# Optimization experiments

Measured on AMD Instinct MI355X. Metric: run time of the kernel, lower is better.

Reference implementation:

```python
import jax, jax.numpy as jnp
import numpy as np

# Fixed genome topology (layered DAG, topologically ordered levels)
B = 4096      # batch
N_IN = 512    # input nodes
H1 = 1536     # hidden level 1
H2 = 1536     # hidden level 2
N_OUT = 512   # output nodes
FAN = 32      # fan-in per non-input node


def setup_inputs() -> dict:
    key = jax.random.key(0)
    ks = jax.random.split(key, 10)
    x = jax.random.normal(ks[0], (B, N_IN), dtype=jnp.float32)
    # level 1: sources among inputs [0, N_IN)
    src0 = jax.random.randint(ks[1], (H1 * FAN,), 0, N_IN, dtype=jnp.int32)
    dst0 = jax.random.randint(ks[2], (H1 * FAN,), 0, H1, dtype=jnp.int32)
    w0 = jax.random.normal(ks[3], (H1 * FAN,), dtype=jnp.float32) * 0.1
    # level 2: sources among inputs + level1 [0, N_IN+H1)
    src1 = jax.random.randint(ks[4], (H2 * FAN,), 0, N_IN + H1, dtype=jnp.int32)
    dst1 = jax.random.randint(ks[5], (H2 * FAN,), 0, H2, dtype=jnp.int32)
    w1 = jax.random.normal(ks[6], (H2 * FAN,), dtype=jnp.float32) * 0.1
    # output level: sources among all earlier nodes [0, N_IN+H1+H2)
    src2 = jax.random.randint(ks[7], (N_OUT * FAN,), 0, N_IN + H1 + H2, dtype=jnp.int32)
    dst2 = jax.random.randint(ks[8], (N_OUT * FAN,), 0, N_OUT, dtype=jnp.int32)
    w2 = jax.random.normal(ks[9], (N_OUT * FAN,), dtype=jnp.float32) * 0.1
    return dict(x=x, src0=src0, dst0=dst0, w0=w0,
                src1=src1, dst1=dst1, w1=w1,
                src2=src2, dst2=dst2, w2=w2)


def _level(node_values, src, dst, w, size):
    # per-edge weighted gather: [B, E]
    vals = node_values[:, src] * w
    # scatter-add into destination nodes of this level: [B, size]
    agg = jnp.zeros((node_values.shape[0], size), node_values.dtype).at[:, dst].add(vals)
    # per-node activation (genome.activation == 'relu'); relu(0)=0 matches
    # original's behavior of leaving unconnected nodes at zero
    return jax.nn.relu(agg)


def reference(x, src0, dst0, w0, src1, dst1, w1, src2, dst2, w2):
    nv = x                                        # [B, N_IN]
    h1 = _level(nv, src0, dst0, w0, H1)           # [B, H1]
    nv = jnp.concatenate([nv, h1], axis=1)        # [B, N_IN+H1]
    h2 = _level(nv, src1, dst1, w1, H2)           # [B, H2]
    nv = jnp.concatenate([nv, h2], axis=1)        # [B, N_IN+H1+H2]
    out = _level(nv, src2, dst2, w2, N_OUT)       # [B, N_OUT]
    return out
```

## Files before the change

kernel.cpp:

```cpp
#include <hip/hip_runtime.h>
#include <hip/hip_fp16.h>
#include <stdint.h>

#define BATCH 4096
#define N_IN  512
#define H1    1536
#define H2    1536
#define N_OUT 512
#define FAN   32
#define E0 (H1 * FAN)
#define E1 (H2 * FAN)
#define E2 (N_OUT * FAN)
#define ETOT (E0 + E1 + E2)
#define NNODES (H1 + H2 + N_OUT)
#define MAXDEG 128

#define ROWU4 520
#define ROWH  (ROWU4 * 8)

#define OFF_EDGES 34078720
#define OFF_CNT   (OFF_EDGES + NNODES * MAXDEG * 8)

__global__ __launch_bounds__(256) void k_transpose_in(const float* __restrict__ x,
                                                      __half* __restrict__ xT) {
    __shared__ float tile[32][33];
    const int tx = threadIdx.x, ty = threadIdx.y;
    const int n0 = blockIdx.x * 32;
    const int b0 = blockIdx.y * 32;
#pragma unroll
    for (int k = 0; k < 32; k += 8)
        tile[ty + k][tx] = x[(size_t)(b0 + ty + k) * N_IN + (n0 + tx)];
    __syncthreads();
#pragma unroll
    for (int k = 0; k < 32; k += 8)
        xT[(size_t)(n0 + ty + k) * ROWH + (b0 + tx)] = __float2half_rn(tile[tx][ty + k]);
}

__global__ __launch_bounds__(256) void k_fill(const int* __restrict__ s0, const int* __restrict__ d0, const float* __restrict__ w0,
                                              const int* __restrict__ s1, const int* __restrict__ d1, const float* __restrict__ w1,
                                              const int* __restrict__ s2, const int* __restrict__ d2, const float* __restrict__ w2,
                                              int* __restrict__ cnt, int2* __restrict__ edges) {
    const int e = blockIdx.x * 256 + threadIdx.x;
    int src, node; float w;
    if (e < E0)           { src = s0[e];          node = d0[e];                w = w0[e]; }
    else if (e < E0 + E1) { int i = e - E0;       src = s1[i]; node = H1 + d1[i];        w = w1[i]; }
    else                  { int i = e - E0 - E1;  src = s2[i]; node = H1 + H2 + d2[i];   w = w2[i]; }
    const int pos = atomicAdd(&cnt[node], 1);
    if (pos < MAXDEG) edges[node * MAXDEG + pos] = make_int2(src, __float_as_int(w));
}

__global__ __launch_bounds__(256, 8)
void k_level(const int2* __restrict__ edges,
             const int* __restrict__ cnt,
             const uint4* __restrict__ nv,
             uint4* __restrict__ outb) {
    const int lane = threadIdx.x & 63;
    const int wv   = threadIdx.x >> 6;
    const int node = __builtin_amdgcn_readfirstlane((blockIdx.y << 2) | wv);
    const int col8 = (blockIdx.x << 6) | lane;

    int c = cnt[node];
    c = (c < 0) ? 0 : (c > MAXDEG ? MAXDEG : c);

    float a0 = 0.f, a1 = 0.f, a2 = 0.f, a3 = 0.f, a4 = 0.f, a5 = 0.f, a6 = 0.f, a7 = 0.f;

#define ACC8(q, W) {                                                    \
    const __half2 h0 = *(const __half2*)&(q).x;                         \
    const __half2 h1 = *(const __half2*)&(q).y;                         \
    const __half2 h2 = *(const __half2*)&(q).z;                         \
    const __half2 h3 = *(const __half2*)&(q).w;                         \
    a0 = fmaf(__low2float(h0),  (W), a0);                               \
    a1 = fmaf(__high2float(h0), (W), a1);                               \
    a2 = fmaf(__low2float(h1),  (W), a2);                               \
    a3 = fmaf(__high2float(h1), (W), a3);                               \
    a4 = fmaf(__low2float(h2),  (W), a4);                               \
    a5 = fmaf(__high2float(h2), (W), a5);                               \
    a6 = fmaf(__low2float(h3),  (W), a6);                               \
    a7 = fmaf(__high2float(h3), (W), a7); }

    for (int base = 0; base < c; base += 64) {
        const int2 my = edges[(size_t)node * MAXDEG + base + lane];
        const int m = (c - base < 64) ? (c - base) : 64;
        int j = 0;
        for (; j + 4 <= m; j += 4) {
            const int   s0i = __builtin_amdgcn_readlane(my.x, j)     & 4095;
            const int   s1i = __builtin_amdgcn_readlane(my.x, j + 1) & 4095;
            const int   s2i = __builtin_amdgcn_readlane(my.x, j + 2) & 4095;
            const int   s3i = __builtin_amdgcn_readlane(my.x, j + 3) & 4095;
            const float wa  = __int_as_float(__builtin_amdgcn_readlane(my.y, j));
            const float wb  = __int_as_float(__builtin_amdgcn_readlane(my.y, j + 1));
            const float wc  = __int_as_float(__builtin_amdgcn_readlane(my.y, j + 2));
            const float wd  = __int_as_float(__builtin_amdgcn_readlane(my.y, j + 3));
            const uint4 q0 = nv[(size_t)s0i * ROWU4 + col8];
            const uint4 q1 = nv[(size_t)s1i * ROWU4 + col8];
            const uint4 q2 = nv[(size_t)s2i * ROWU4 + col8];
            const uint4 q3 = nv[(size_t)s3i * ROWU4 + col8];
            ACC8(q0, wa);
            ACC8(q1, wb);
            ACC8(q2, wc);
            ACC8(q3, wd);
        }
        for (; j < m; ++j) {
            const int   s0i = __builtin_amdgcn_readlane(my.x, j) & 4095;
            const float wa  = __int_as_float(__builtin_amdgcn_readlane(my.y, j));
            const uint4 q0 = nv[(size_t)s0i * ROWU4 + col8];
            ACC8(q0, wa);
        }
    }
#undef ACC8

    a0 = fmaxf(a0, 0.f); a1 = fmaxf(a1, 0.f); a2 = fmaxf(a2, 0.f); a3 = fmaxf(a3, 0.f);
    a4 = fmaxf(a4, 0.f); a5 = fmaxf(a5, 0.f); a6 = fmaxf(a6, 0.f); a7 = fmaxf(a7, 0.f);

    const __half2 h0 = __floats2half2_rn(a0, a1);
    const __half2 h1 = __floats2half2_rn(a2, a3);
    const __half2 h2 = __floats2half2_rn(a4, a5);
    const __half2 h3 = __floats2half2_rn(a6, a7);
    uint4 p;
    p.x = *(const uint32_t*)&h0; p.y = *(const uint32_t*)&h1;
    p.z = *(const uint32_t*)&h2; p.w = *(const uint32_t*)&h3;
    outb[(size_t)node * ROWU4 + col8] = p;
}

__global__ __launch_bounds__(256) void k_transpose_out(const __half* __restrict__ outh,
                                                       float* __restrict__ out) {
    __shared__ float tile[32][33];
    const int tx = threadIdx.x, ty = threadIdx.y;
    const int n0 = blockIdx.x * 32;
    const int b0 = blockIdx.y * 32;
#pragma unroll
    for (int k = 0; k < 32; k += 8)
        tile[ty + k][tx] = __half2float(outh[(size_t)(n0 + ty + k) * ROWH + (b0 + tx)]);
    __syncthreads();
#pragma unroll
    for (int k = 0; k < 32; k += 8)
        out[(size_t)(b0 + ty + k) * N_OUT + (n0 + tx)] = tile[tx][ty + k];
}

extern "C" void kernel_launch(void* const* d_in, const int* in_sizes, int n_in,
                              void* d_out, int out_size, void* d_ws, size_t ws_size,
                              hipStream_t stream) {
    const float* x  = (const float*)d_in[0];
    const int* s0   = (const int*)d_in[1];
    const int* dd0  = (const int*)d_in[2];
    const float* w0 = (const float*)d_in[3];
    const int* s1   = (const int*)d_in[4];
    const int* dd1  = (const int*)d_in[5];
    const float* w1 = (const float*)d_in[6];
    const int* s2   = (const int*)d_in[7];
    const int* dd2  = (const int*)d_in[8];
    const float* w2 = (const float*)d_in[9];

    char* ws        = (char*)d_ws;
    uint4*    nv4   = (uint4*)ws;
    int2*     edges = (int2*)(ws + OFF_EDGES);
    int*      cnt   = (int*)(ws + OFF_CNT);

    hipMemsetAsync(cnt, 0, NNODES * sizeof(int), stream);
    k_fill<<<ETOT / 256, 256, 0, stream>>>(s0, dd0, w0, s1, dd1, w1, s2, dd2, w2, cnt, edges);

    k_transpose_in<<<dim3(N_IN / 32, BATCH / 32), dim3(32, 8), 0, stream>>>(x, (__half*)ws);

    k_level<<<dim3(8, H1 / 4), 256, 0, stream>>>(edges, cnt, nv4,
                                                 nv4 + (size_t)N_IN * ROWU4);
    k_level<<<dim3(8, H2 / 4), 256, 0, stream>>>(edges + (size_t)H1 * MAXDEG, cnt + H1, nv4,
                                                 nv4 + (size_t)(N_IN + H1) * ROWU4);
    k_level<<<dim3(8, N_OUT / 4), 256, 0, stream>>>(edges + (size_t)(H1 + H2) * MAXDEG, cnt + H1 + H2, nv4,
                                                    nv4 + (size_t)(N_IN + H1 + H2) * ROWU4);

    k_transpose_out<<<dim3(N_OUT / 32, BATCH / 32), dim3(32, 8), 0, stream>>>(
        (const __half*)(ws + (size_t)(N_IN + H1 + H2) * ROWH * 2), (float*)d_out);
}
```

Measured before the change: 145.5 us.

## Stream gathered node rows through LDS with async global_load_lds pipeline

Replaces the direct per-edge register gathers in the level kernel with asynchronous global-to-LDS loads, one LDS slot per in-flight edge, four edges deep. Each edge is consumed after a manual vmcnt wait and its slot is refilled right away, so gather latency overlaps with the FMA work. Edges beyond the first 64, and any remainder not divisible by 4, fall back to plain scalar loads. The risks are the hand-written waitcnt correctness, extra LDS traffic, and the serial tail loop.

```diff
diff --git a/kernel.cpp b/kernel.cpp
--- a/kernel.cpp
+++ b/kernel.cpp
@@ -54,6 +54,7 @@
              const int* __restrict__ cnt,
              const uint4* __restrict__ nv,
              uint4* __restrict__ outb) {
+    __shared__ uint4 sh[4][4][64];
     const int lane = threadIdx.x & 63;
     const int wv   = threadIdx.x >> 6;
     const int node = __builtin_amdgcn_readfirstlane((blockIdx.y << 2) | wv);
@@ -78,35 +79,62 @@
     a6 = fmaf(__low2float(h3),  (W), a6);                               \
     a7 = fmaf(__high2float(h3), (W), a7); }
 
-    for (int base = 0; base < c; base += 64) {
-        const int2 my = edges[(size_t)node * MAXDEG + base + lane];
-        const int m = (c - base < 64) ? (c - base) : 64;
+#define GLD(K, SRC)                                                                   \
+    __builtin_amdgcn_global_load_lds(                                                 \
+        (const __attribute__((address_space(1))) void*)(const void*)                  \
+            (nv + (size_t)(SRC) * ROWU4 + col8),                                      \
+        (__attribute__((address_space(3))) void*)(void*)(&sh[wv][K][0]), 16, 0, 0)
+
+#define CONS(K, J, WAITSTR) {                                                         \
+    asm volatile(WAITSTR ::: "memory");                                               \
+    __builtin_amdgcn_sched_barrier(0);                                                \
+    const uint4 q = sh[wv][K][lane];                                                  \
+    const float w = __int_as_float(__builtin_amdgcn_readlane(my.y, (J) + (K)));       \
+    ACC8(q, w);                                                                       \
+    __builtin_amdgcn_sched_barrier(0);                                                \
+}
+
+#define REISS(K, J) {                                                                 \
+    const int s = __builtin_amdgcn_readlane(my.x, (J) + 4 + (K)) & 4095;              \
+    GLD(K, s);                                                                        \
+}
+
+    const int nfull = ((c > 64) ? 64 : c) & ~3;
+
+    if (nfull >= 4) {
+        const int2 my = edges[(size_t)node * MAXDEG + lane];
+
+        {
+            const int sa = __builtin_amdgcn_readlane(my.x, 0) & 4095;
+            const int sb = __builtin_amdgcn_readlane(my.x, 1) & 4095;
+            const int sc = __builtin_amdgcn_readlane(my.x, 2) & 4095;
+            const int sd = __builtin_amdgcn_readlane(my.x, 3) & 4095;
+            GLD(0, sa); GLD(1, sb); GLD(2, sc); GLD(3, sd);
+        }
+
         int j = 0;
-        for (; j + 4 <= m; j += 4) {
-            const int   s0i = __builtin_amdgcn_readlane(my.x, j)     & 4095;
-            const int   s1i = __builtin_amdgcn_readlane(my.x, j + 1) & 4095;
-            const int   s2i = __builtin_amdgcn_readlane(my.x, j + 2) & 4095;
-            const int   s3i = __builtin_amdgcn_readlane(my.x, j + 3) & 4095;
-            const float wa  = __int_as_float(__builtin_amdgcn_readlane(my.y, j));
-            const float wb  = __int_as_float(__builtin_amdgcn_readlane(my.y, j + 1));
-            const float wc  = __int_as_float(__builtin_amdgcn_readlane(my.y, j + 2));
-            const float wd  = __int_as_float(__builtin_amdgcn_readlane(my.y, j + 3));
-            const uint4 q0 = nv[(size_t)s0i * ROWU4 + col8];
-            const uint4 q1 = nv[(size_t)s1i * ROWU4 + col8];
-            const uint4 q2 = nv[(size_t)s2i * ROWU4 + col8];
-            const uint4 q3 = nv[(size_t)s3i * ROWU4 + col8];
-            ACC8(q0, wa);
-            ACC8(q1, wb);
-            ACC8(q2, wc);
-            ACC8(q3, wd);
+        for (; j + 8 <= nfull; j += 4) {
+            CONS(0, j, "s_waitcnt vmcnt(3)") REISS(0, j)
+            CONS(1, j, "s_waitcnt vmcnt(3)") REISS(1, j)
+            CONS(2, j, "s_waitcnt vmcnt(3)") REISS(2, j)
+            CONS(3, j, "s_waitcnt vmcnt(3)") REISS(3, j)
         }
-        for (; j < m; ++j) {
-            const int   s0i = __builtin_amdgcn_readlane(my.x, j) & 4095;
-            const float wa  = __int_as_float(__builtin_amdgcn_readlane(my.y, j));
-            const uint4 q0 = nv[(size_t)s0i * ROWU4 + col8];
-            ACC8(q0, wa);
-        }
+        CONS(0, j, "s_waitcnt vmcnt(3)")
+        CONS(1, j, "s_waitcnt vmcnt(2)")
+        CONS(2, j, "s_waitcnt vmcnt(1)")
+        CONS(3, j, "s_waitcnt vmcnt(0)")
     }
+
+    for (int t = nfull; t < c; ++t) {
+        const int2 e = edges[(size_t)node * MAXDEG + t];
+        const int   s = e.x & 4095;
+        const float w = __int_as_float(e.y);
+        const uint4 q = nv[(size_t)s * ROWU4 + col8];
+        ACC8(q, w);
+    }
+#undef REISS
+#undef CONS
+#undef GLD
 #undef ACC8
 
     a0 = fmaxf(a0, 0.f); a1 = fmaxf(a1, 0.f); a2 = fmaxf(a2, 0.f); a3 = fmaxf(a3, 0.f);
```

Result: slower. 160.6 us (+10.4%).
